# Kernel tuning notes

Measured on AMD Instinct MI355X. Metric: run time of the kernel, lower is better.

Reference implementation:

```python
import jax, jax.numpy as jnp
import numpy as np

NUM_HEADS = 16
MAX_FREQ = 10.0
LN_EPS = 1e-5
PI = float(np.pi)


def layer_norm(x, w, b):
    mu = jnp.mean(x, axis=-1, keepdims=True)
    var = jnp.mean(jnp.square(x - mu), axis=-1, keepdims=True)
    return (x - mu) * jax.lax.rsqrt(var + LN_EPS) * w + b


def rotate_half(x):
    # interleaved pairs: (x0,x1,x2,x3,...) -> (-x1,x0,-x3,x2,...)
    x1 = x[..., 0::2]
    x2 = x[..., 1::2]
    return jnp.stack((-x2, x1), axis=-1).reshape(x.shape)


def drofe(q, k, freqband, demo):
    # q, k: [B,H,N,D]; freqband: [N,2] (lower/upper band bound); demo: [B,2] (age, gender)
    D = q.shape[-1]
    freqs = jnp.linspace(1.0, MAX_FREQ / 2.0, D // 4).astype(q.dtype) * PI  # [D/4]
    ang = jnp.concatenate([freqband[:, 0:1] * freqs, freqband[:, 1:2] * freqs], axis=-1)  # [N, D/2]
    ang = jnp.repeat(ang, 2, axis=-1)  # [N, D]
    cos, sin = jnp.cos(ang), jnp.sin(ang)
    age = demo[:, 0][:, None, None, None]
    gender = demo[:, 1][:, None, None, None]
    q = q * cos * age + rotate_half(q) * sin * gender
    k = k * cos * age + rotate_half(k) * sin * gender
    return q, k


def setup_inputs() -> dict:
    key = jax.random.key(0)
    ks = jax.random.split(key, 16)
    B, N, C, F = 8, 1024, 1024, 4096
    s = 0.02
    return {
        "x": jax.random.normal(ks[0], (B, N, C), jnp.float32),
        "demographic_info": jax.random.uniform(ks[1], (B, 2), jnp.float32),
        "explanation": jax.random.normal(ks[2], (B, N, C), jnp.float32),
        "freqband": jax.random.uniform(ks[3], (N, 2), jnp.float32) * 50.0,
        "w_qkv": jax.random.normal(ks[4], (C, 3 * C), jnp.float32) * s,
        "w_proj": jax.random.normal(ks[5], (C, C), jnp.float32) * s,
        "b_proj": jnp.zeros((C,), jnp.float32),
        "gamma1": jnp.full((C,), 1e-5, jnp.float32),
        "gamma2": jnp.full((C,), 1e-5, jnp.float32),
        "ln1_w": jnp.ones((C,), jnp.float32),
        "ln1_b": jnp.zeros((C,), jnp.float32),
        "ln2_w": jnp.ones((C,), jnp.float32),
        "ln2_b": jnp.zeros((C,), jnp.float32),
        "w1": jax.random.normal(ks[6], (C, F), jnp.float32) * s,
        "b1": jnp.zeros((F,), jnp.float32),
        "w2": jax.random.normal(ks[7], (F, C), jnp.float32) * s,
        "b2": jnp.zeros((C,), jnp.float32),
    }


def reference(x, demographic_info, explanation, freqband, w_qkv, w_proj, b_proj,
              gamma1, gamma2, ln1_w, ln1_b, ln2_w, ln2_b, w1, b1, w2, b2):
    B, N, C = x.shape
    H = NUM_HEADS
    D = C // H

    def split_qkv(t):
        return (t @ w_qkv).reshape(B, N, 3, H, D).transpose(2, 0, 3, 1, 4)  # [3,B,H,N,D]

    v = split_qkv(x)[2]
    qkv_e = split_qkv(explanation)  # explanation-swap: q,k come from explanation
    q, k = qkv_e[0], qkv_e[1]
    q, k = drofe(q, k, freqband, demographic_info)

    attn = jax.nn.softmax(jnp.einsum('bhnd,bhmd->bhnm', q, k) * (D ** -0.5), axis=-1)
    o = jnp.einsum('bhnm,bhmd->bhnd', attn, v).transpose(0, 2, 1, 3).reshape(B, N, C)
    o = o @ w_proj + b_proj

    x = layer_norm(x + gamma1 * o, ln1_w, ln1_b)  # post-norm + LayerScale
    h = jax.nn.gelu(x @ w1 + b1, approximate=False) @ w2 + b2
    x = layer_norm(x + gamma2 * h, ln2_w, ln2_b)
    return x
```

## Files before the change

kernel.cpp:

```cpp
#include <hip/hip_runtime.h>
#include <hip/hip_bf16.h>
#include <math.h>

typedef __attribute__((ext_vector_type(8))) short bf16x8;
typedef __attribute__((ext_vector_type(8))) unsigned short u16x8;
typedef __attribute__((ext_vector_type(4))) float f32x4;
typedef __attribute__((ext_vector_type(4))) unsigned short u16x4;

__device__ inline unsigned short f2bf(float f) {
    union { float f; unsigned u; } v; v.f = f;
    unsigned r = (v.u + 0x7fff + ((v.u >> 16) & 1)) >> 16;
    return (unsigned short)r;
}
__device__ inline float bf2f(unsigned short u) {
    union { unsigned u; float f; } v; v.u = ((unsigned)u) << 16; return v.f;
}

#define GLL16(gp, lp) __builtin_amdgcn_global_load_lds(                      \
    (const __attribute__((address_space(1))) void*)(gp),                     \
    (__attribute__((address_space(3))) void*)(lp), 16, 0, 0)

template<int EPI, int OUT_BF>
__global__ __launch_bounds__(256, 4) void gemm2ph128(
    const unsigned short* __restrict__ A,
    const unsigned short* __restrict__ Bt,
    const float* __restrict__ bias,
    void* __restrict__ Cout,
    void* __restrict__ Cout2,
    const float* __restrict__ fbq,
    const float* __restrict__ demo,
    int M, int Nn, int K, int ldc)
{
    __shared__ unsigned char lds[2][16384];
    const int tid = threadIdx.x;
    const int w = tid >> 6, lane = tid & 63;
    const int lk = lane & 15, lg = lane >> 4;
    const int wr = w >> 1, wc = w & 1;
    const int nbn = Nn >> 7;
    const int nb = gridDim.x;
    int bid = blockIdx.x;
    int swz = (nb & 7) ? bid : (bid & 7) * (nb >> 3) + (bid >> 3);
    const int bm = (swz / nbn) << 7, bn = (swz % nbn) << 7;

    f32x4 acc[4][4] = {};

    auto stage = [&](int buf, int k0) {
        #pragma unroll
        for (int i = 0; i < 4; ++i) {
            int s = tid + i * 256;
            int r = s >> 2, c = s & 3;
            int cs = (c ^ r ^ (r >> 2)) & 3;
            const unsigned short* gp = (r < 128)
                ? A  + (size_t)(bm + r) * K + k0 + cs * 8
                : Bt + (size_t)(bn + (r - 128)) * K + k0 + cs * 8;
            GLL16(gp, &lds[buf][s * 16]);
        }
    };

    const int NT = K >> 5;
    stage(0, 0);
    __syncthreads();
    int cur = 0;
    for (int t = 0; t < NT; ++t) {
        if (t + 1 < NT) stage(cur ^ 1, (t + 1) << 5);
        bf16x8 af[4], bfr[4];
        #pragma unroll
        for (int m = 0; m < 4; ++m) {
            int row = wr * 64 + m * 16 + lk;
            int sl = (lg ^ row ^ (row >> 2)) & 3;
            af[m] = *(const bf16x8*)&lds[cur][row * 64 + sl * 16];
        }
        #pragma unroll
        for (int n = 0; n < 4; ++n) {
            int row = wc * 64 + n * 16 + lk;
            int sl = (lg ^ row ^ (row >> 2)) & 3;
            bfr[n] = *(const bf16x8*)&lds[cur][8192 + row * 64 + sl * 16];
        }
        #pragma unroll
        for (int m = 0; m < 4; ++m)
            #pragma unroll
            for (int n = 0; n < 4; ++n)
                acc[m][n] = __builtin_amdgcn_mfma_f32_16x16x32_bf16(af[m], bfr[n], acc[m][n], 0, 0, 0);
        __syncthreads();
        cur ^= 1;
    }

    if (EPI == 3) {
        const float PI_F = 3.14159265358979323846f;
        const int b_ = bm >> 10;
        const float age = demo[b_ * 2 + 0], gen = demo[b_ * 2 + 1];
        #pragma unroll
        for (int m = 0; m < 4; ++m) {
            #pragma unroll
            for (int n = 0; n < 4; ++n) {
                int col = bn + wc * 64 + n * 16 + lk;
                int i = (col & 63) >> 1;
                int ii = (i < 16) ? i : i - 16;
                float freq = (1.0f + (float)ii * (4.0f / 15.0f)) * PI_F;
                int fsel = (i >= 16) ? 1 : 0;
                #pragma unroll
                for (int r = 0; r < 4; ++r) {
                    int row = bm + wr * 64 + m * 16 + lg * 4 + r;
                    float val = acc[m][n][r];
                    float par = __shfl_xor(val, 1);
                    int nn = row & 1023;
                    float ang = fbq[nn * 2 + fsel] * freq;
                    float sv, cv;
                    __sincosf(ang, &sv, &cv);
                    float ca = cv * age, sg = sv * gen;
                    float res = (col & 1) ? (val * ca + par * sg)
                                          : (val * ca - par * sg);
                    if (col < 1024)
                        ((unsigned short*)Cout)[(size_t)row * 1024 + col] = f2bf(res * 0.125f);
                    else
                        ((unsigned short*)Cout2)[(size_t)row * 1024 + col - 1024] = f2bf(res);
                }
            }
        }
        return;
    }

    #pragma unroll
    for (int m = 0; m < 4; ++m) {
        int row = bm + wr * 64 + m * 16 + lg * 4;
        #pragma unroll
        for (int n = 0; n < 4; ++n) {
            int col = bn + wc * 64 + n * 16 + lk;
            #pragma unroll
            for (int r = 0; r < 4; ++r) {
                float v = acc[m][n][r];
                if (EPI >= 1) v += bias[col];
                if (EPI == 2) {
                    float u = v * 0.7978845608f * (1.0f + 0.044715f * v * v);
                    v = v / (1.0f + __expf(-2.0f * u));
                }
                if (OUT_BF)
                    ((unsigned short*)Cout)[(size_t)(row + r) * ldc + col] = f2bf(v);
                else
                    ((float*)Cout)[(size_t)(row + r) * ldc + col] = v;
            }
        }
    }
}

__global__ __launch_bounds__(256) void cvt_bf16(
    const float* __restrict__ src, unsigned short* __restrict__ dst, int n)
{
    int i = (blockIdx.x * 256 + threadIdx.x) * 4;
    if (i < n) {
        float4 v = *(const float4*)(src + i);
        u16x4 o = { f2bf(v.x), f2bf(v.y), f2bf(v.z), f2bf(v.w) };
        *(u16x4*)(dst + i) = o;
    }
}

__global__ __launch_bounds__(256) void transpose_cvt(
    const float* __restrict__ src, unsigned short* __restrict__ dst, int R, int Cc)
{
    __shared__ float t[32][33];
    const int bc = blockIdx.x * 32, br = blockIdx.y * 32;
    const int tx = threadIdx.x & 31, ty = threadIdx.x >> 5;
    #pragma unroll
    for (int i = 0; i < 4; ++i)
        t[ty + i * 8][tx] = src[(size_t)(br + ty + i * 8) * Cc + bc + tx];
    __syncthreads();
    #pragma unroll
    for (int i = 0; i < 4; ++i)
        dst[(size_t)(bc + ty + i * 8) * R + br + tx] = f2bf(t[tx][ty + i * 8]);
}

__global__ __launch_bounds__(256, 4) void attn_mfma(
    const unsigned short* __restrict__ Q, const unsigned short* __restrict__ K,
    const unsigned short* __restrict__ V, unsigned short* __restrict__ O,
    int B, int H, int N)
{
    __shared__ unsigned short Ks[64 * 64];
    __shared__ unsigned short Vt[64 * 72];
    __shared__ unsigned short Ps[4][16 * 72];

    const int bi = blockIdx.x;
    const int bh = (bi & 7) + 8 * ((bi >> 3) & 15);
    const int q0 = (bi >> 7) * 128;
    const int b = bh >> 4, h = bh & 15;
    const int tid = threadIdx.x;
    const int w = tid >> 6, lane = tid & 63;
    const int lg = lane >> 4, lk = lane & 15;

    bf16x8 qf[2][2];
    #pragma unroll
    for (int qt = 0; qt < 2; ++qt) {
        const unsigned short* qrow =
            Q + (size_t)(b * N + q0 + qt * 64 + w * 16 + lk) * 1024 + h * 64;
        qf[qt][0] = *(const bf16x8*)(qrow + lg * 8);
        qf[qt][1] = *(const bf16x8*)(qrow + 32 + lg * 8);
    }

    f32x4 o[2][4] = {};
    float m_run[2] = { -INFINITY, -INFINITY }, l_run[2] = { 0.f, 0.f };

    for (int t0 = 0; t0 < N; t0 += 64) {
        const size_t kvbase = (size_t)(b * N + t0) * 1024 + h * 64;
        #pragma unroll
        for (int it = 0; it < 2; ++it) {
            int s = it * 256 + tid;
            int row = s >> 3, cb = (s & 7) << 4;
            int dby = cb ^ ((row & 7) << 4);
            GLL16(K + kvbase + (size_t)row * 1024 + (dby >> 1), &Ks[s * 8]);
        }
        {
            int c = tid >> 5, k0 = (tid & 31) * 2;
            const unsigned short* vp = V + kvbase + (size_t)k0 * 1024 + c * 8;
            u16x8 va = *(const u16x8*)vp;
            u16x8 vb = *(const u16x8*)(vp + 1024);
            #pragma unroll
            for (int j = 0; j < 8; ++j) {
                unsigned val = (unsigned)va[j] | ((unsigned)vb[j] << 16);
                *(unsigned*)&Vt[(c * 8 + j) * 72 + k0] = val;
            }
        }
        __syncthreads();

        #pragma unroll
        for (int qt = 0; qt < 2; ++qt) {
            f32x4 s4[4];
            __builtin_amdgcn_s_setprio(1);
            #pragma unroll
            for (int sub = 0; sub < 4; ++sub) {
                f32x4 acc = {0.f, 0.f, 0.f, 0.f};
                #pragma unroll
                for (int kh = 0; kh < 2; ++kh) {
                    int cc = (kh * 64 + lg * 16) ^ ((lk & 7) << 4);
                    bf16x8 kf = *(const bf16x8*)&Ks[(sub * 16 + lk) * 64 + (cc >> 1)];
                    acc = __builtin_amdgcn_mfma_f32_16x16x32_bf16(kf, qf[qt][kh], acc, 0, 0, 0);
                }
                s4[sub] = acc;
            }
            __builtin_amdgcn_s_setprio(0);

            float pmax = -INFINITY;
            #pragma unroll
            for (int sub = 0; sub < 4; ++sub)
                #pragma unroll
                for (int r = 0; r < 4; ++r) pmax = fmaxf(pmax, s4[sub][r]);
            pmax = fmaxf(pmax, __shfl_xor(pmax, 16));
            pmax = fmaxf(pmax, __shfl_xor(pmax, 32));

            if (!__all(pmax - m_run[qt] <= 8.0f)) {
                float mn = fmaxf(m_run[qt], pmax);
                float corr = __expf(m_run[qt] - mn);
                m_run[qt] = mn;
                l_run[qt] *= corr;
                #pragma unroll
                for (int ds = 0; ds < 4; ++ds)
                    #pragma unroll
                    for (int r = 0; r < 4; ++r) o[qt][ds][r] *= corr;
            }

            float psum = 0.f;
            unsigned pw[4][2];
            #pragma unroll
            for (int sub = 0; sub < 4; ++sub) {
                float p0 = __expf(s4[sub][0] - m_run[qt]);
                float p1 = __expf(s4[sub][1] - m_run[qt]);
                float p2 = __expf(s4[sub][2] - m_run[qt]);
                float p3 = __expf(s4[sub][3] - m_run[qt]);
                psum += (p0 + p1) + (p2 + p3);
                pw[sub][0] = (__float_as_uint(p0) >> 16) | (__float_as_uint(p1) & 0xffff0000u);
                pw[sub][1] = (__float_as_uint(p2) >> 16) | (__float_as_uint(p3) & 0xffff0000u);
            }
            psum += __shfl_xor(psum, 16);
            psum += __shfl_xor(psum, 32);
            l_run[qt] += psum;
            #pragma unroll
            for (int sub = 0; sub < 4; ++sub) {
                *(unsigned*)&Ps[w][lk * 72 + sub * 16 + lg * 4]     = pw[sub][0];
                *(unsigned*)&Ps[w][lk * 72 + sub * 16 + lg * 4 + 2] = pw[sub][1];
            }
            asm volatile("s_waitcnt lgkmcnt(0)" ::: "memory");

            __builtin_amdgcn_s_setprio(1);
            #pragma unroll
            for (int kh = 0; kh < 2; ++kh) {
                bf16x8 pf = *(const bf16x8*)&Ps[w][lk * 72 + kh * 32 + lg * 8];
                #pragma unroll
                for (int ds = 0; ds < 4; ++ds) {
                    bf16x8 vf = *(const bf16x8*)&Vt[(ds * 16 + lk) * 72 + kh * 32 + lg * 8];
                    o[qt][ds] = __builtin_amdgcn_mfma_f32_16x16x32_bf16(vf, pf, o[qt][ds], 0, 0, 0);
                }
            }
            __builtin_amdgcn_s_setprio(0);
        }
        __syncthreads();
    }

    #pragma unroll
    for (int qt = 0; qt < 2; ++qt) {
        unsigned short* orow =
            O + (size_t)(b * N + q0 + qt * 64 + w * 16 + lk) * 1024 + h * 64;
        float rinv = 1.0f / l_run[qt];
        #pragma unroll
        for (int ds = 0; ds < 4; ++ds) {
            u16x4 pk = { f2bf(o[qt][ds][0] * rinv), f2bf(o[qt][ds][1] * rinv),
                         f2bf(o[qt][ds][2] * rinv), f2bf(o[qt][ds][3] * rinv) };
            *(u16x4*)(orow + ds * 16 + lg * 4) = pk;
        }
    }
}

__global__ __launch_bounds__(256) void ln_res_kernel(
    const float* __restrict__ x, const unsigned short* __restrict__ y,
    const float* __restrict__ gamma, const float* __restrict__ w,
    const float* __restrict__ bia, float* __restrict__ out,
    unsigned short* __restrict__ out_bf, int C)
{
    const int row = blockIdx.x;
    __shared__ float buf[1024];
    __shared__ float red[8];
    const size_t base = (size_t)row * C;
    float s = 0.f, ss = 0.f;
    for (int c = threadIdx.x; c < C; c += 256) {
        float v = x[base + c] + gamma[c] * bf2f(y[base + c]);
        buf[c] = v; s += v; ss += v * v;
    }
    #pragma unroll
    for (int msk = 1; msk < 64; msk <<= 1) { s += __shfl_xor(s, msk); ss += __shfl_xor(ss, msk); }
    int wv = threadIdx.x >> 6, lane = threadIdx.x & 63;
    if (lane == 0) { red[wv * 2] = s; red[wv * 2 + 1] = ss; }
    __syncthreads();
    if (threadIdx.x == 0) {
        float S = 0.f, SS = 0.f;
        #pragma unroll
        for (int i = 0; i < 4; ++i) { S += red[2 * i]; SS += red[2 * i + 1]; }
        red[0] = S; red[1] = SS;
    }
    __syncthreads();
    float mu = red[0] / C;
    float var = red[1] / C - mu * mu;
    float rstd = rsqrtf(var + 1e-5f);
    for (int c = threadIdx.x; c < C; c += 256) {
        float v = (buf[c] - mu) * rstd * w[c] + bia[c];
        out[base + c] = v;
        if (out_bf) out_bf[base + c] = f2bf(v);
    }
}

extern "C" void kernel_launch(void* const* d_in, const int* in_sizes, int n_in,
                              void* d_out, int out_size, void* d_ws, size_t ws_size,
                              hipStream_t stream)
{
    const float* x      = (const float*)d_in[0];
    const float* demo   = (const float*)d_in[1];
    const float* expl   = (const float*)d_in[2];
    const float* fb     = (const float*)d_in[3];
    const float* w_qkv  = (const float*)d_in[4];
    const float* w_proj = (const float*)d_in[5];
    const float* b_proj = (const float*)d_in[6];
    const float* gamma1 = (const float*)d_in[7];
    const float* gamma2 = (const float*)d_in[8];
    const float* ln1_w  = (const float*)d_in[9];
    const float* ln1_b  = (const float*)d_in[10];
    const float* ln2_w  = (const float*)d_in[11];
    const float* ln2_b  = (const float*)d_in[12];
    const float* w1     = (const float*)d_in[13];
    const float* b1     = (const float*)d_in[14];
    const float* w2     = (const float*)d_in[15];
    const float* b2     = (const float*)d_in[16];
    float* out = (float*)d_out;

    const int B = 8, N = 1024, C = 1024, F = 4096, H = 16;
    const int M = B * N;
    const size_t Mi = 1048576;

    float* ws = (float*)d_ws;
    unsigned short* Obf  = (unsigned short*)ws;
    unsigned short* H2   = (unsigned short*)ws;
    unsigned short* Qbf  = (unsigned short*)(ws + 8 * Mi);
    unsigned short* Kbf  = (unsigned short*)(ws + 12 * Mi);
    unsigned short* Vbf  = (unsigned short*)(ws + 16 * Mi);
    unsigned short* Hid  = (unsigned short*)(ws + 8 * Mi);
    unsigned short* Ebf  = (unsigned short*)(ws + 24 * Mi);
    unsigned short* Xbf  = (unsigned short*)(ws + 28 * Mi);
    unsigned short* Pb   = (unsigned short*)(ws + 24 * Mi);
    float*          X1   = ws + 32 * Mi;
    unsigned short* X1bf = (unsigned short*)(ws + 40 * Mi);
    unsigned short* Wt   = (unsigned short*)(ws + 44 * Mi);
    unsigned short* wqkvT  = Wt;
    unsigned short* wprojT = Wt + (size_t)3145728;
    unsigned short* w1T    = wprojT + (size_t)1048576;
    unsigned short* w2T    = w1T + (size_t)4194304;

    dim3 blk(256);
    const int MC = M * C;

    hipLaunchKernelGGL(cvt_bf16, dim3(MC / 1024), blk, 0, stream, expl, Ebf, MC);
    hipLaunchKernelGGL(cvt_bf16, dim3(MC / 1024), blk, 0, stream, x, Xbf, MC);
    hipLaunchKernelGGL(transpose_cvt, dim3(96, 32), blk, 0, stream, w_qkv, wqkvT, C, 3 * C);
    hipLaunchKernelGGL(transpose_cvt, dim3(32, 32), blk, 0, stream, w_proj, wprojT, C, C);
    hipLaunchKernelGGL(transpose_cvt, dim3(128, 32), blk, 0, stream, w1, w1T, C, F);
    hipLaunchKernelGGL(transpose_cvt, dim3(32, 128), blk, 0, stream, w2, w2T, F, C);

    hipLaunchKernelGGL((gemm2ph128<3,1>), dim3(64 * 16), blk, 0, stream, Ebf, wqkvT,
                       (const float*)nullptr, (void*)Qbf, (void*)Kbf, fb, demo, M, 2048, C, 2048);
    hipLaunchKernelGGL((gemm2ph128<0,1>), dim3(64 * 8), blk, 0, stream, Xbf,
                       wqkvT + (size_t)2048 * 1024, (const float*)nullptr, (void*)Vbf,
                       (void*)nullptr, (const float*)nullptr, (const float*)nullptr, M, 1024, C, 1024);

    hipLaunchKernelGGL(attn_mfma, dim3(B * H * (N / 128)), blk, 0, stream, Qbf, Kbf, Vbf, Obf, B, H, N);

    hipLaunchKernelGGL((gemm2ph128<1,1>), dim3(64 * 8), blk, 0, stream, Obf, wprojT, b_proj,
                       (void*)Pb, (void*)nullptr, (const float*)nullptr, (const float*)nullptr, M, 1024, C, 1024);

    hipLaunchKernelGGL(ln_res_kernel, dim3(M), blk, 0, stream, x, Pb, gamma1, ln1_w, ln1_b, X1, X1bf, C);

    hipLaunchKernelGGL((gemm2ph128<2,1>), dim3(64 * 32), blk, 0, stream, X1bf, w1T, b1,
                       (void*)Hid, (void*)nullptr, (const float*)nullptr, (const float*)nullptr, M, F, C, F);
    hipLaunchKernelGGL((gemm2ph128<1,1>), dim3(64 * 8), blk, 0, stream, Hid, w2T, b2,
                       (void*)H2, (void*)nullptr, (const float*)nullptr, (const float*)nullptr, M, 1024, F, 1024);

    hipLaunchKernelGGL(ln_res_kernel, dim3(M), blk, 0, stream, X1, H2, gamma2, ln2_w, ln2_b, out, (unsigned short*)nullptr, C);
}
```

Baseline: 409.0 us.

## Split-K the proj and FFN2 GEMMs, reducing partial sums inside layernorm

The projection and second FFN GEMMs now split K in half across twice as many blocks. Each half writes its own bf16 partial output, with bias added only once, and the layernorm-residual kernel sums the two partials. The goal is better CU occupancy and load balance for these narrow-N GEMMs. The second layernorm now reads the residual from the bf16 copy instead of an fp32 buffer, which removes one fp32 write and read but costs precision. The extra partial buffer and bf16 rounding of each partial add traffic and error.

```diff
diff --git a/kernel.cpp b/kernel.cpp
--- a/kernel.cpp
+++ b/kernel.cpp
@@ -20,7 +20,7 @@
     (const __attribute__((address_space(1))) void*)(gp),                     \
     (__attribute__((address_space(3))) void*)(lp), 16, 0, 0)
 
-template<int EPI, int OUT_BF>
+template<int EPI, int OUT_BF, int SPLITK>
 __global__ __launch_bounds__(256, 4) void gemm2ph128(
     const unsigned short* __restrict__ A,
     const unsigned short* __restrict__ Bt,
@@ -37,8 +37,17 @@
     const int lk = lane & 15, lg = lane >> 4;
     const int wr = w >> 1, wc = w & 1;
     const int nbn = Nn >> 7;
-    const int nb = gridDim.x;
+    int nb = gridDim.x;
     int bid = blockIdx.x;
+    int koff = 0, Keff = K;
+    bool sk = false;
+    if (SPLITK) {
+        int nbt = nb >> 1;
+        sk = bid >= nbt;
+        if (sk) { bid -= nbt; koff = K >> 1; }
+        Keff = K >> 1;
+        nb = nbt;
+    }
     int swz = (nb & 7) ? bid : (bid & 7) * (nb >> 3) + (bid >> 3);
     const int bm = (swz / nbn) << 7, bn = (swz % nbn) << 7;
 
@@ -51,13 +60,13 @@
             int r = s >> 2, c = s & 3;
             int cs = (c ^ r ^ (r >> 2)) & 3;
             const unsigned short* gp = (r < 128)
-                ? A  + (size_t)(bm + r) * K + k0 + cs * 8
-                : Bt + (size_t)(bn + (r - 128)) * K + k0 + cs * 8;
+                ? A  + (size_t)(bm + r) * K + koff + k0 + cs * 8
+                : Bt + (size_t)(bn + (r - 128)) * K + koff + k0 + cs * 8;
             GLL16(gp, &lds[buf][s * 16]);
         }
     };
 
-    const int NT = K >> 5;
+    const int NT = Keff >> 5;
     stage(0, 0);
     __syncthreads();
     int cur = 0;
@@ -120,6 +129,7 @@
         return;
     }
 
+    void* outp = (SPLITK && sk) ? Cout2 : Cout;
     #pragma unroll
     for (int m = 0; m < 4; ++m) {
         int row = bm + wr * 64 + m * 16 + lg * 4;
@@ -129,15 +139,15 @@
             #pragma unroll
             for (int r = 0; r < 4; ++r) {
                 float v = acc[m][n][r];
-                if (EPI >= 1) v += bias[col];
+                if (EPI >= 1 && !sk) v += bias[col];
                 if (EPI == 2) {
                     float u = v * 0.7978845608f * (1.0f + 0.044715f * v * v);
                     v = v / (1.0f + __expf(-2.0f * u));
                 }
                 if (OUT_BF)
-                    ((unsigned short*)Cout)[(size_t)(row + r) * ldc + col] = f2bf(v);
+                    ((unsigned short*)outp)[(size_t)(row + r) * ldc + col] = f2bf(v);
                 else
-                    ((float*)Cout)[(size_t)(row + r) * ldc + col] = v;
+                    ((float*)outp)[(size_t)(row + r) * ldc + col] = v;
             }
         }
     }
@@ -307,8 +317,10 @@
     }
 }
 
-__global__ __launch_bounds__(256) void ln_res_kernel(
-    const float* __restrict__ x, const unsigned short* __restrict__ y,
+template<int XBF, int Y2>
+__global__ __launch_bounds__(256) void ln_res3(
+    const void* __restrict__ xv, const unsigned short* __restrict__ y1,
+    const unsigned short* __restrict__ y2,
     const float* __restrict__ gamma, const float* __restrict__ w,
     const float* __restrict__ bia, float* __restrict__ out,
     unsigned short* __restrict__ out_bf, int C)
@@ -319,7 +331,11 @@
     const size_t base = (size_t)row * C;
     float s = 0.f, ss = 0.f;
     for (int c = threadIdx.x; c < C; c += 256) {
-        float v = x[base + c] + gamma[c] * bf2f(y[base + c]);
+        float xf = XBF ? bf2f(((const unsigned short*)xv)[base + c])
+                       : ((const float*)xv)[base + c];
+        float yy = bf2f(y1[base + c]);
+        if (Y2) yy += bf2f(y2[base + c]);
+        float v = xf + gamma[c] * yy;
         buf[c] = v; s += v; ss += v * v;
     }
     #pragma unroll
@@ -339,7 +355,7 @@
     float rstd = rsqrtf(var + 1e-5f);
     for (int c = threadIdx.x; c < C; c += 256) {
         float v = (buf[c] - mu) * rstd * w[c] + bia[c];
-        out[base + c] = v;
+        if (out) out[base + c] = v;
         if (out_bf) out_bf[base + c] = f2bf(v);
     }
 }
@@ -373,7 +389,8 @@
 
     float* ws = (float*)d_ws;
     unsigned short* Obf  = (unsigned short*)ws;
-    unsigned short* H2   = (unsigned short*)ws;
+    unsigned short* H2a  = (unsigned short*)ws;
+    unsigned short* H2b  = (unsigned short*)(ws + 4 * Mi);
     unsigned short* Qbf  = (unsigned short*)(ws + 8 * Mi);
     unsigned short* Kbf  = (unsigned short*)(ws + 12 * Mi);
     unsigned short* Vbf  = (unsigned short*)(ws + 16 * Mi);
@@ -381,7 +398,7 @@
     unsigned short* Ebf  = (unsigned short*)(ws + 24 * Mi);
     unsigned short* Xbf  = (unsigned short*)(ws + 28 * Mi);
     unsigned short* Pb   = (unsigned short*)(ws + 24 * Mi);
-    float*          X1   = ws + 32 * Mi;
+    unsigned short* Pb2  = (unsigned short*)(ws + 28 * Mi);
     unsigned short* X1bf = (unsigned short*)(ws + 40 * Mi);
     unsigned short* Wt   = (unsigned short*)(ws + 44 * Mi);
     unsigned short* wqkvT  = Wt;
@@ -399,23 +416,25 @@
     hipLaunchKernelGGL(transpose_cvt, dim3(128, 32), blk, 0, stream, w1, w1T, C, F);
     hipLaunchKernelGGL(transpose_cvt, dim3(32, 128), blk, 0, stream, w2, w2T, F, C);
 
-    hipLaunchKernelGGL((gemm2ph128<3,1>), dim3(64 * 16), blk, 0, stream, Ebf, wqkvT,
+    hipLaunchKernelGGL((gemm2ph128<3,1,0>), dim3(64 * 16), blk, 0, stream, Ebf, wqkvT,
                        (const float*)nullptr, (void*)Qbf, (void*)Kbf, fb, demo, M, 2048, C, 2048);
-    hipLaunchKernelGGL((gemm2ph128<0,1>), dim3(64 * 8), blk, 0, stream, Xbf,
+    hipLaunchKernelGGL((gemm2ph128<0,1,0>), dim3(64 * 8), blk, 0, stream, Xbf,
                        wqkvT + (size_t)2048 * 1024, (const float*)nullptr, (void*)Vbf,
                        (void*)nullptr, (const float*)nullptr, (const float*)nullptr, M, 1024, C, 1024);
 
     hipLaunchKernelGGL(attn_mfma, dim3(B * H * (N / 128)), blk, 0, stream, Qbf, Kbf, Vbf, Obf, B, H, N);
 
-    hipLaunchKernelGGL((gemm2ph128<1,1>), dim3(64 * 8), blk, 0, stream, Obf, wprojT, b_proj,
-                       (void*)Pb, (void*)nullptr, (const float*)nullptr, (const float*)nullptr, M, 1024, C, 1024);
-
-    hipLaunchKernelGGL(ln_res_kernel, dim3(M), blk, 0, stream, x, Pb, gamma1, ln1_w, ln1_b, X1, X1bf, C);
-
-    hipLaunchKernelGGL((gemm2ph128<2,1>), dim3(64 * 32), blk, 0, stream, X1bf, w1T, b1,
+    hipLaunchKernelGGL((gemm2ph128<1,1,1>), dim3(64 * 16), blk, 0, stream, Obf, wprojT, b_proj,
+                       (void*)Pb, (void*)Pb2, (const float*)nullptr, (const float*)nullptr, M, 1024, C, 1024);
+
+    hipLaunchKernelGGL((ln_res3<0,1>), dim3(M), blk, 0, stream, (const void*)x, Pb, Pb2,
+                       gamma1, ln1_w, ln1_b, (float*)nullptr, X1bf, C);
+
+    hipLaunchKernelGGL((gemm2ph128<2,1,0>), dim3(64 * 32), blk, 0, stream, X1bf, w1T, b1,
                        (void*)Hid, (void*)nullptr, (const float*)nullptr, (const float*)nullptr, M, F, C, F);
-    hipLaunchKernelGGL((gemm2ph128<1,1>), dim3(64 * 8), blk, 0, stream, Hid, w2T, b2,
-                       (void*)H2, (void*)nullptr, (const float*)nullptr, (const float*)nullptr, M, 1024, F, 1024);
-
-    hipLaunchKernelGGL(ln_res_kernel, dim3(M), blk, 0, stream, X1, H2, gamma2, ln2_w, ln2_b, out, (unsigned short*)nullptr, C);
-}
+    hipLaunchKernelGGL((gemm2ph128<1,1,1>), dim3(64 * 16), blk, 0, stream, Hid, w2T, b2,
+                       (void*)H2a, (void*)H2b, (const float*)nullptr, (const float*)nullptr, M, 1024, F, 1024);
+
+    hipLaunchKernelGGL((ln_res3<1,1>), dim3(M), blk, 0, stream, (const void*)X1bf, H2a, H2b,
+                       gamma2, ln2_w, ln2_b, out, (unsigned short*)nullptr, C);
+}
```

Measured after the change: 422.5 us. 1.03x slower.
